# Kernel optimization log

Hardware: AMD Instinct MI355X
Metric: run time of the kernel (lower is better)

## Reference

```python
import jax, jax.numpy as jnp
import numpy as np

B, T, S, C, HS = 4, 4096, 4096, 1024, 64

def setup_inputs() -> dict:
    key = jax.random.key(0)
    k1, k2, k3, k4, k5 = jax.random.split(key, 5)
    x = jax.random.normal(k1, (B, T, C), dtype=jnp.float32)
    encode_out = jax.random.normal(k2, (B, S, C), dtype=jnp.float32)
    # nn.Linear(C, HS, bias=False): weight [HS, C]; store transposed [C, HS] for x @ W
    sc = 1.0 / np.sqrt(C)
    Wk = jax.random.uniform(k3, (C, HS), dtype=jnp.float32, minval=-sc, maxval=sc)
    Wq = jax.random.uniform(k4, (C, HS), dtype=jnp.float32, minval=-sc, maxval=sc)
    Wv = jax.random.uniform(k5, (C, HS), dtype=jnp.float32, minval=-sc, maxval=sc)
    return {"x": x, "encode_out": encode_out, "Wq": Wq, "Wk": Wk, "Wv": Wv}

def reference(x, encode_out, Wq, Wk, Wv):
    # Single-head cross-attention (mask=False path)
    q = x @ Wq                      # [B, T, HS]
    k = encode_out @ Wk             # [B, S, HS]
    v = encode_out @ Wv             # [B, S, HS]
    scale = k.shape[-1] ** -0.5
    wei = jnp.einsum('btd,bsd->bts', q, k) * scale   # [B, T, S]
    wei = jax.nn.softmax(wei, axis=-1)
    out = jnp.einsum('bts,bsd->btd', wei, v)         # [B, T, HS]
    return out
```

## Files before the change

kernel.cpp:

```cpp
#include <hip/hip_runtime.h>
#include <hip/hip_bf16.h>

#define TT 4096
#define SS 4096
#define CC 1024
#define HS 64

typedef __bf16 bf16x8 __attribute__((ext_vector_type(8)));
typedef __bf16 bf16x4 __attribute__((ext_vector_type(4)));
typedef float  f32x4  __attribute__((ext_vector_type(4)));
typedef float  f32x16 __attribute__((ext_vector_type(16)));

#define MFMA16(A,B,C) __builtin_amdgcn_mfma_f32_16x16x32_bf16((A),(B),(C),0,0,0)
#define MFMA32(A,B,C) __builtin_amdgcn_mfma_f32_32x32x16_bf16((A),(B),(C),0,0,0)

__device__ __forceinline__ int pkbf(float a, float b) {
    union { struct { __bf16 lo, hi; } h; int i; } u;
    u.h.lo = (__bf16)a; u.h.hi = (__bf16)b;
    return u.i;
}

__device__ __forceinline__ bf16x8 cvt8(float4 f0, float4 f1) {
    bf16x8 a;
    a[0] = (__bf16)f0.x; a[1] = (__bf16)f0.y; a[2] = (__bf16)f0.z; a[3] = (__bf16)f0.w;
    a[4] = (__bf16)f1.x; a[5] = (__bf16)f1.y; a[6] = (__bf16)f1.z; a[7] = (__bf16)f1.w;
    return a;
}

__device__ __forceinline__ void gload_lds16(const void* g, char* l) {
    __builtin_amdgcn_global_load_lds(
        (const __attribute__((address_space(1))) void*)g,
        (__attribute__((address_space(3))) void*)l, 16, 0, 0);
}

__global__ __launch_bounds__(256) void prep_wt(const float* __restrict__ Wq,
                                               const float* __restrict__ Wk,
                                               const float* __restrict__ Wv,
                                               __bf16* __restrict__ wt) {
    int idx = blockIdx.x * 256 + threadIdx.x;
    int mat = idx >> 16;
    int e   = idx & 65535;
    int d   = e >> 10;
    int kk  = e & 1023;
    const float* W = (mat == 0) ? Wq : (mat == 1 ? Wk : Wv);
    float v = W[kk * HS + d];
    if (mat == 0) v *= 0.125f * 1.44269504088896340736f;
    wt[idx] = (__bf16)v;
}

__global__ __launch_bounds__(256, 2) void proj_qkv(const float* __restrict__ x,
                                                   const float* __restrict__ enc,
                                                   const __bf16* __restrict__ wt,
                                                   __bf16* __restrict__ qb,
                                                   __bf16* __restrict__ kb,
                                                   __bf16* __restrict__ vt) {
    __shared__ char smem[65536];
    int tid = threadIdx.x;
    int w = tid >> 6, l = tid & 63, lq = l >> 4, lm = l & 15;
    int kv   = blockIdx.x & 1;
    int row0 = (blockIdx.x >> 1) * 64;
    int rowbase = row0 + w * 16;
    const float*  src   = kv ? enc : x;
    const __bf16* wbase = wt + (kv ? HS * CC : 0);
    const __bf16* wvb   = wt + 2 * HS * CC;

    #define STAGE_A(k, p) do {                                                          \
        _Pragma("unroll")                                                               \
        for (int j = 0; j < 4; ++j) {                                                   \
            int rloc = j * 4 + (l >> 4);                                                \
            int gs = (l & 15) ^ rloc;                                                   \
            gload_lds16(src + (size_t)(rowbase + rloc) * CC + (k) * 64 + gs * 4,        \
                        smem + (p) * 16384 + w * 4096 + j * 1024);                      \
        }                                                                               \
    } while (0)

    #define STAGE_B1(k, p, mptr, moff) do {                                             \
        _Pragma("unroll")                                                               \
        for (int i = 0; i < 2; ++i) {                                                   \
            int rrel = i * 32 + w * 8 + (l >> 3);                                       \
            int gs = (l & 7) ^ (rrel & 7);                                              \
            gload_lds16(mptr + (size_t)rrel * CC + (k) * 64 + gs * 8,                   \
                        smem + 32768 + (p) * 16384 + (moff) + i * 4096 + w * 1024);     \
        }                                                                               \
    } while (0)

    f32x4 accA[4], accV[4];
    #pragma unroll
    for (int i = 0; i < 4; i++) { accA[i] = (f32x4){0.f,0.f,0.f,0.f}; accV[i] = (f32x4){0.f,0.f,0.f,0.f}; }

    if (kv) {
        STAGE_A(0, 0); STAGE_B1(0, 0, wbase, 0); STAGE_B1(0, 0, wvb, 8192);
        #pragma unroll
        for (int k = 0; k < 16; ++k) {
            int p = k & 1;
            if (k < 15) {
                STAGE_A(k + 1, p ^ 1);
                STAGE_B1(k + 1, p ^ 1, wbase, 0);
                STAGE_B1(k + 1, p ^ 1, wvb, 8192);
                asm volatile("s_waitcnt vmcnt(8)\ns_barrier" ::: "memory");
            } else {
                asm volatile("s_waitcnt vmcnt(0)\ns_barrier" ::: "memory");
            }
            const char* Ab = smem + p * 16384 + w * 4096;
            const char* Bb = smem + 32768 + p * 16384;
            #pragma unroll
            for (int ks = 0; ks < 2; ++ks) {
                int g0 = ks * 8 + lq * 2;
                float4 f0 = *(const float4*)(Ab + lm * 256 + ((g0)     ^ lm) * 16);
                float4 f1 = *(const float4*)(Ab + lm * 256 + ((g0 + 1) ^ lm) * 16);
                bf16x8 af = cvt8(f0, f1);
                int bg = ((ks * 4 + lq) ^ (lm & 7)) * 16;
                #pragma unroll
                for (int nt = 0; nt < 4; nt++) {
                    bf16x8 bA = *(const bf16x8*)(Bb + (nt * 16 + lm) * 128 + bg);
                    bf16x8 bV = *(const bf16x8*)(Bb + 8192 + (nt * 16 + lm) * 128 + bg);
                    accA[nt] = MFMA16(af, bA, accA[nt]);
                    accV[nt] = MFMA16(af, bV, accV[nt]);
                }
            }
            asm volatile("s_waitcnt lgkmcnt(0)\ns_barrier" ::: "memory");
        }
    } else {
        STAGE_A(0, 0); STAGE_B1(0, 0, wbase, 0);
        #pragma unroll
        for (int k = 0; k < 16; ++k) {
            int p = k & 1;
            if (k < 15) {
                STAGE_A(k + 1, p ^ 1);
                STAGE_B1(k + 1, p ^ 1, wbase, 0);
                asm volatile("s_waitcnt vmcnt(6)\ns_barrier" ::: "memory");
            } else {
                asm volatile("s_waitcnt vmcnt(0)\ns_barrier" ::: "memory");
            }
            const char* Ab = smem + p * 16384 + w * 4096;
            const char* Bb = smem + 32768 + p * 16384;
            #pragma unroll
            for (int ks = 0; ks < 2; ++ks) {
                int g0 = ks * 8 + lq * 2;
                float4 f0 = *(const float4*)(Ab + lm * 256 + ((g0)     ^ lm) * 16);
                float4 f1 = *(const float4*)(Ab + lm * 256 + ((g0 + 1) ^ lm) * 16);
                bf16x8 af = cvt8(f0, f1);
                int bg = ((ks * 4 + lq) ^ (lm & 7)) * 16;
                #pragma unroll
                for (int nt = 0; nt < 4; nt++) {
                    bf16x8 bA = *(const bf16x8*)(Bb + (nt * 16 + lm) * 128 + bg);
                    accA[nt] = MFMA16(af, bA, accA[nt]);
                }
            }
            asm volatile("s_waitcnt lgkmcnt(0)\ns_barrier" ::: "memory");
        }
    }
    #undef STAGE_A
    #undef STAGE_B1

    {
        __bf16* dstA = kv ? kb : qb;
        #pragma unroll
        for (int nt = 0; nt < 4; nt++)
            #pragma unroll
            for (int r = 0; r < 4; r++)
                dstA[(size_t)(rowbase + lq * 4 + r) * HS + nt * 16 + lm] = (__bf16)accA[nt][r];
    }
    if (kv) {
        int bb = row0 >> 12;
        int sbase = (row0 & 4095) + w * 16 + lq * 4;
        #pragma unroll
        for (int nt = 0; nt < 4; nt++) {
            bf16x4 pk = { (__bf16)accV[nt][0], (__bf16)accV[nt][1],
                          (__bf16)accV[nt][2], (__bf16)accV[nt][3] };
            *(bf16x4*)(vt + ((size_t)bb * HS + nt * 16 + lm) * SS + sbase) = pk;
        }
    }
}

__global__ __launch_bounds__(512, 1) void attn(const __bf16* __restrict__ qb,
                                               const __bf16* __restrict__ kb,
                                               const __bf16* __restrict__ vt,
                                               float* __restrict__ out) {
    extern __shared__ char smem[];
    int tid = threadIdx.x, w = tid >> 6, l = tid & 63;
    int hi = l >> 5, ln = l & 31;
    int qg = w & 1, ss = w >> 1;

    int bid = blockIdx.x;
    int b = bid & 3, tb = bid >> 2;
    int t0 = tb * 64;

    const __bf16* qp = qb + ((size_t)(b * TT + t0 + qg * 32 + ln)) * HS + hi * 8;
    bf16x8 qf[4];
    qf[0] = *(const bf16x8*)(qp);
    qf[1] = *(const bf16x8*)(qp + 16);
    qf[2] = *(const bf16x8*)(qp + 32);
    qf[3] = *(const bf16x8*)(qp + 48);

    const __bf16* kbase = kb + (size_t)b * SS * HS;
    const __bf16* vbase = vt + (size_t)b * HS * SS;

    #define STAGE(t, p) do {                                                            \
        _Pragma("unroll")                                                               \
        for (int i = 0; i < 4; ++i) {                                                   \
            int idx = i * 512 + tid;                                                    \
            int sr = idx >> 3, g = idx & 7;                                             \
            gload_lds16(kbase + ((size_t)(t) * 256 + sr) * 64 + ((g ^ (sr & 7)) * 8),   \
                        smem + (p) * 65536 + idx * 16);                                 \
        }                                                                               \
        _Pragma("unroll")                                                               \
        for (int i = 0; i < 4; ++i) {                                                   \
            int idx = i * 512 + tid;                                                    \
            int dr = idx >> 5, g = idx & 31;                                            \
            gload_lds16(vbase + (size_t)dr * SS + (t) * 256 + ((g ^ (dr & 7)) * 8),     \
                        smem + (p) * 65536 + 32768 + idx * 16);                         \
        }                                                                               \
    } while (0)

    f32x16 oacc0, oacc1;
    #pragma unroll
    for (int i = 0; i < 16; i++) { oacc0[i] = 0.f; oacc1[i] = 0.f; }
    float lsum = 0.f;

    STAGE(0, 0);
    for (int t = 0; t < 16; ++t) {
        int p = t & 1;
        if (t < 15) {
            STAGE(t + 1, p ^ 1);
            asm volatile("s_waitcnt vmcnt(8)\ns_barrier" ::: "memory");
        } else {
            asm volatile("s_waitcnt vmcnt(0)\ns_barrier" ::: "memory");
        }
        const char* Kb = smem + p * 65536;
        const char* Vb = smem + p * 65536 + 32768;

        #pragma unroll
        for (int sg = 0; sg < 2; ++sg) {
            int srow = ss * 64 + sg * 32 + ln;
            bf16x8 ka[4];
            #pragma unroll
            for (int ks = 0; ks < 4; ++ks)
                ka[ks] = *(const bf16x8*)(Kb + srow * 128 + (((ks * 2 + hi) ^ (srow & 7)) * 16));

            f32x16 s;
            #pragma unroll
            for (int i = 0; i < 16; i++) s[i] = 0.f;
            s = MFMA32(ka[0], qf[0], s);
            s = MFMA32(ka[1], qf[1], s);
            s = MFMA32(ka[2], qf[2], s);
            s = MFMA32(ka[3], qf[3], s);

            float pv[16];
            #pragma unroll
            for (int i = 0; i < 16; i++) pv[i] = __builtin_amdgcn_exp2f(s[i]);
            float l0 = (pv[0] + pv[1]) + (pv[2] + pv[3]);
            float l1 = (pv[4] + pv[5]) + (pv[6] + pv[7]);
            float l2 = (pv[8] + pv[9]) + (pv[10] + pv[11]);
            float l3 = (pv[12] + pv[13]) + (pv[14] + pv[15]);
            lsum += (l0 + l1) + (l2 + l3);

            int d01 = pkbf(pv[0],  pv[1]),  d23 = pkbf(pv[2],  pv[3]);
            int d45 = pkbf(pv[4],  pv[5]),  d67 = pkbf(pv[6],  pv[7]);
            int e01 = pkbf(pv[8],  pv[9]),  e23 = pkbf(pv[10], pv[11]);
            int e45 = pkbf(pv[12], pv[13]), e67 = pkbf(pv[14], pv[15]);
            asm("v_permlane32_swap_b32 %0, %1" : "+v"(d01), "+v"(d45));
            asm("v_permlane32_swap_b32 %0, %1" : "+v"(d23), "+v"(d67));
            asm("v_permlane32_swap_b32 %0, %1" : "+v"(e01), "+v"(e45));
            asm("v_permlane32_swap_b32 %0, %1" : "+v"(e23), "+v"(e67));
            union F { int i[4]; bf16x8 v; } f0, f1;
            f0.i[0] = d01; f0.i[1] = d23; f0.i[2] = d45; f0.i[3] = d67;
            f1.i[0] = e01; f1.i[1] = e23; f1.i[2] = e45; f1.i[3] = e67;

            int ksp = ss * 4 + sg * 2;
            #pragma unroll
            for (int dg = 0; dg < 2; ++dg) {
                int d = dg * 32 + ln;
                bf16x8 va0 = *(const bf16x8*)(Vb + d * 512 + ((((ksp)     * 2 + hi) ^ (d & 7)) * 16));
                bf16x8 va1 = *(const bf16x8*)(Vb + d * 512 + ((((ksp + 1) * 2 + hi) ^ (d & 7)) * 16));
                if (dg == 0) { oacc0 = MFMA32(va0, f0.v, oacc0); oacc0 = MFMA32(va1, f1.v, oacc0); }
                else         { oacc1 = MFMA32(va0, f0.v, oacc1); oacc1 = MFMA32(va1, f1.v, oacc1); }
            }
        }
        asm volatile("s_waitcnt lgkmcnt(0)\ns_barrier" ::: "memory");
    }
    #undef STAGE

    lsum += __shfl_xor(lsum, 32, 64);

    float* accC = (float*)smem;
    float* lsC  = (float*)(smem + 102400);
    union O { f32x16 v; f32x4 q[4]; } o0, o1;
    o0.v = oacc0; o1.v = oacc1;
    {
        int b0 = ((qg * 4 + ss) * 2 + 0) * 1280 + l * 20;
        int b1 = ((qg * 4 + ss) * 2 + 1) * 1280 + l * 20;
        #pragma unroll
        for (int g = 0; g < 4; ++g) {
            *(f32x4*)&accC[b0 + g * 4] = o0.q[g];
            *(f32x4*)&accC[b1 + g * 4] = o1.q[g];
        }
        if (l < 32) lsC[(qg * 4 + ss) * 32 + l] = lsum;
    }
    __syncthreads();

    {
        int q = tid >> 3, c8 = tid & 7;
        int qg2 = q >> 5, ln2 = q & 31;
        float ls = 0.f;
        #pragma unroll
        for (int s2 = 0; s2 < 4; ++s2) ls += lsC[(qg2 * 4 + s2) * 32 + ln2];
        float inv = 1.0f / ls;
        float vout[8];
        #pragma unroll
        for (int j = 0; j < 8; ++j) {
            int d = c8 * 8 + j;
            int hi2 = (d >> 2) & 1, dg = d >> 5;
            int r = (((d & 31) >> 3) << 2) | (d & 3);
            float sum = 0.f;
            #pragma unroll
            for (int s2 = 0; s2 < 4; ++s2)
                sum += accC[((qg2 * 4 + s2) * 2 + dg) * 1280 + (hi2 * 32 + ln2) * 20 + r];
            vout[j] = sum * inv;
        }
        float* orow = out + (size_t)(b * TT + t0 + q) * HS + c8 * 8;
        *(f32x4*)(orow)     = *(f32x4*)&vout[0];
        *(f32x4*)(orow + 4) = *(f32x4*)&vout[4];
    }
}

extern "C" void kernel_launch(void* const* d_in, const int* in_sizes, int n_in,
                              void* d_out, int out_size, void* d_ws, size_t ws_size,
                              hipStream_t stream) {
    (void)in_sizes; (void)n_in; (void)out_size; (void)ws_size;
    const float* x   = (const float*)d_in[0];
    const float* enc = (const float*)d_in[1];
    const float* Wq  = (const float*)d_in[2];
    const float* Wk  = (const float*)d_in[3];
    const float* Wv  = (const float*)d_in[4];
    float* out = (float*)d_out;

    char* ws = (char*)d_ws;
    __bf16* wtb  = (__bf16*)ws;
    __bf16* qbuf = (__bf16*)(ws + 393216);
    __bf16* kbuf = (__bf16*)(ws + 393216 + 2097152);
    __bf16* vbuf = (__bf16*)(ws + 393216 + 2 * 2097152);

    hipLaunchKernelGGL(prep_wt,  dim3(768), dim3(256), 0, stream, Wq, Wk, Wv, wtb);
    hipLaunchKernelGGL(proj_qkv, dim3(512), dim3(256), 0, stream, x, enc, wtb, qbuf, kbuf, vbuf);
    hipLaunchKernelGGL(attn,     dim3(256), dim3(512), 131072, stream, qbuf, kbuf, vbuf, out);
}
```

Baseline: 65.78 us.

## Use 512-thread projection blocks with triple-buffered activation staging

```diff
diff --git a/kernel.cpp b/kernel.cpp
--- a/kernel.cpp
+++ b/kernel.cpp
@@ -48,40 +48,36 @@
     wt[idx] = (__bf16)v;
 }
 
-__global__ __launch_bounds__(256, 2) void proj_qkv(const float* __restrict__ x,
+__global__ __launch_bounds__(512, 1) void proj_qkv(const float* __restrict__ x,
                                                    const float* __restrict__ enc,
                                                    const __bf16* __restrict__ wt,
                                                    __bf16* __restrict__ qb,
                                                    __bf16* __restrict__ kb,
                                                    __bf16* __restrict__ vt) {
-    __shared__ char smem[65536];
+    extern __shared__ char smem[];
     int tid = threadIdx.x;
     int w = tid >> 6, l = tid & 63, lq = l >> 4, lm = l & 15;
     int kv   = blockIdx.x & 1;
-    int row0 = (blockIdx.x >> 1) * 64;
+    int row0 = (blockIdx.x >> 1) * 128;
     int rowbase = row0 + w * 16;
     const float*  src   = kv ? enc : x;
     const __bf16* wbase = wt + (kv ? HS * CC : 0);
     const __bf16* wvb   = wt + 2 * HS * CC;
 
-    #define STAGE_A(k, p) do {                                                          \
+    #define STAGE_A(k) do {                                                             \
         _Pragma("unroll")                                                               \
         for (int j = 0; j < 4; ++j) {                                                   \
             int rloc = j * 4 + (l >> 4);                                                \
             int gs = (l & 15) ^ rloc;                                                   \
             gload_lds16(src + (size_t)(rowbase + rloc) * CC + (k) * 64 + gs * 4,        \
-                        smem + (p) * 16384 + w * 4096 + j * 1024);                      \
+                        smem + ((k) % 3) * 32768 + w * 4096 + j * 1024);                \
         }                                                                               \
     } while (0)
 
-    #define STAGE_B1(k, p, mptr, moff) do {                                             \
-        _Pragma("unroll")                                                               \
-        for (int i = 0; i < 2; ++i) {                                                   \
-            int rrel = i * 32 + w * 8 + (l >> 3);                                       \
-            int gs = (l & 7) ^ (rrel & 7);                                              \
-            gload_lds16(mptr + (size_t)rrel * CC + (k) * 64 + gs * 8,                   \
-                        smem + 32768 + (p) * 16384 + (moff) + i * 4096 + w * 1024);     \
-        }                                                                               \
+    #define STAGE_B(k, mptr, moff) do {                                                 \
+        int gs = (l & 7) ^ (l >> 3);                                                    \
+        gload_lds16(mptr + (size_t)(w * 8 + (l >> 3)) * CC + (k) * 64 + gs * 8,         \
+                    smem + 98304 + ((k) & 1) * 16384 + (moff) + w * 1024);              \
     } while (0)
 
     f32x4 accA[4], accV[4];
@@ -89,20 +85,18 @@
     for (int i = 0; i < 4; i++) { accA[i] = (f32x4){0.f,0.f,0.f,0.f}; accV[i] = (f32x4){0.f,0.f,0.f,0.f}; }
 
     if (kv) {
-        STAGE_A(0, 0); STAGE_B1(0, 0, wbase, 0); STAGE_B1(0, 0, wvb, 8192);
+        STAGE_B(0, wbase, 0); STAGE_B(0, wvb, 8192);
+        STAGE_A(0); STAGE_A(1);
         #pragma unroll
         for (int k = 0; k < 16; ++k) {
-            int p = k & 1;
-            if (k < 15) {
-                STAGE_A(k + 1, p ^ 1);
-                STAGE_B1(k + 1, p ^ 1, wbase, 0);
-                STAGE_B1(k + 1, p ^ 1, wvb, 8192);
-                asm volatile("s_waitcnt vmcnt(8)\ns_barrier" ::: "memory");
-            } else {
-                asm volatile("s_waitcnt vmcnt(0)\ns_barrier" ::: "memory");
-            }
-            const char* Ab = smem + p * 16384 + w * 4096;
-            const char* Bb = smem + 32768 + p * 16384;
+            if (k < 15) { STAGE_B(k + 1, wbase, 0); STAGE_B(k + 1, wvb, 8192); }
+            if (k < 14) STAGE_A(k + 2);
+            if (k < 14)      asm volatile("s_waitcnt vmcnt(10)\ns_barrier" ::: "memory");
+            else if (k == 14) asm volatile("s_waitcnt vmcnt(6)\ns_barrier" ::: "memory");
+            else              asm volatile("s_waitcnt vmcnt(0)\ns_barrier" ::: "memory");
+
+            const char* Ab = smem + (k % 3) * 32768 + w * 4096;
+            const char* Bb = smem + 98304 + (k & 1) * 16384;
             #pragma unroll
             for (int ks = 0; ks < 2; ++ks) {
                 int g0 = ks * 8 + lq * 2;
@@ -121,19 +115,18 @@
             asm volatile("s_waitcnt lgkmcnt(0)\ns_barrier" ::: "memory");
         }
     } else {
-        STAGE_A(0, 0); STAGE_B1(0, 0, wbase, 0);
+        STAGE_B(0, wbase, 0);
+        STAGE_A(0); STAGE_A(1);
         #pragma unroll
         for (int k = 0; k < 16; ++k) {
-            int p = k & 1;
-            if (k < 15) {
-                STAGE_A(k + 1, p ^ 1);
-                STAGE_B1(k + 1, p ^ 1, wbase, 0);
-                asm volatile("s_waitcnt vmcnt(6)\ns_barrier" ::: "memory");
-            } else {
-                asm volatile("s_waitcnt vmcnt(0)\ns_barrier" ::: "memory");
-            }
-            const char* Ab = smem + p * 16384 + w * 4096;
-            const char* Bb = smem + 32768 + p * 16384;
+            if (k < 15) STAGE_B(k + 1, wbase, 0);
+            if (k < 14) STAGE_A(k + 2);
+            if (k < 14)      asm volatile("s_waitcnt vmcnt(9)\ns_barrier" ::: "memory");
+            else if (k == 14) asm volatile("s_waitcnt vmcnt(5)\ns_barrier" ::: "memory");
+            else              asm volatile("s_waitcnt vmcnt(0)\ns_barrier" ::: "memory");
+
+            const char* Ab = smem + (k % 3) * 32768 + w * 4096;
+            const char* Bb = smem + 98304 + (k & 1) * 16384;
             #pragma unroll
             for (int ks = 0; ks < 2; ++ks) {
                 int g0 = ks * 8 + lq * 2;
@@ -151,7 +144,7 @@
         }
     }
     #undef STAGE_A
-    #undef STAGE_B1
+    #undef STAGE_B
 
     {
         __bf16* dstA = kv ? kb : qb;
@@ -341,7 +334,7 @@
     __bf16* kbuf = (__bf16*)(ws + 393216 + 2097152);
     __bf16* vbuf = (__bf16*)(ws + 393216 + 2 * 2097152);
 
-    hipLaunchKernelGGL(prep_wt,  dim3(768), dim3(256), 0, stream, Wq, Wk, Wv, wtb);
-    hipLaunchKernelGGL(proj_qkv, dim3(512), dim3(256), 0, stream, x, enc, wtb, qbuf, kbuf, vbuf);
+    hipLaunchKernelGGL(prep_wt,  dim3(768), dim3(256), 0,      stream, Wq, Wk, Wv, wtb);
+    hipLaunchKernelGGL(proj_qkv, dim3(256), dim3(512), 131072, stream, x, enc, wtb, qbuf, kbuf, vbuf);
     hipLaunchKernelGGL(attn,     dim3(256), dim3(512), 131072, stream, qbuf, kbuf, vbuf, out);
 }
```

Result: no change. 65.12 us (-1.0%).
